# Performance work log

Hardware: AMD Instinct MI355X
Metric: run time of the kernel (lower is better)

## Reference

```python
import jax, jax.numpy as jnp
import numpy as np
import math

B, D, NH, NS, NT = 16, 256, 512, 8, 32
NV = NS * NT          # 256 prediction variables
L, H, A = 4, 8, 64    # attention layers, heads, head dim
HA = H * A            # 512
M = 512               # mlp_dim
R = 128               # resolution
EPS = 1e-5


def setup_inputs() -> dict:
    key = jax.random.key(0)
    ks = jax.random.split(key, 32)
    s = 0.02
    inp = {
        'hist_encoded': jax.random.normal(ks[0], (B, NH, D), jnp.float32),
        'hist_true_u': jax.random.uniform(ks[1], (B, NH), jnp.float32),
        'pred_encoded': jax.random.normal(ks[2], (B, NV, D), jnp.float32),
        'pred_true_u': jax.random.uniform(ks[3], (B, NV), jnp.float32),
        # dimension shifting layer
        'ds_w': jax.random.normal(ks[4], (D, HA), jnp.float32) * s,
        'ds_b': jnp.zeros((HA,), jnp.float32),
        # per-layer, per-head key/value creators: Linear(D+1 -> A)
        'key_w': jax.random.normal(ks[5], (L, H, D + 1, A), jnp.float32) * s,
        'key_b': jnp.zeros((L, H, A), jnp.float32),
        'val_w': jax.random.normal(ks[6], (L, H, D + 1, A), jnp.float32) * s,
        'val_b': jnp.zeros((L, H, A), jnp.float32),
        # layer norms
        'ln1_g': jnp.ones((L, HA), jnp.float32),
        'ln1_b': jnp.zeros((L, HA), jnp.float32),
        'ln2_g': jnp.ones((L, HA), jnp.float32),
        'ln2_b': jnp.zeros((L, HA), jnp.float32),
        # feed-forward (mlp_layers=2): HA->M, M->M, M->HA
        'ff_w1': jax.random.normal(ks[7], (L, HA, M), jnp.float32) * s,
        'ff_b1': jnp.zeros((L, M), jnp.float32),
        'ff_w2': jax.random.normal(ks[8], (L, M, M), jnp.float32) * s,
        'ff_b2': jnp.zeros((L, M), jnp.float32),
        'ff_w3': jax.random.normal(ks[9], (L, M, HA), jnp.float32) * s,
        'ff_b3': jnp.zeros((L, HA), jnp.float32),
        # dist extractor
        'de_w': jax.random.normal(ks[10], (HA, R), jnp.float32) * s,
        'de_b': jnp.zeros((R,), jnp.float32),
        'num_series': NS,
        'num_timesteps': NT,
    }
    return inp


def _ln(x, g, b):
    m = x.mean(-1, keepdims=True)
    v = ((x - m) ** 2).mean(-1, keepdims=True)
    return g * (x - m) / jnp.sqrt(v + EPS) + b


def _forward(hist_encoded, hist_true_u, pred_encoded, pred_true_u,
             ds_w, ds_b, key_w, key_b, val_w, val_b,
             ln1_g, ln1_b, ln2_g, ln2_b,
             ff_w1, ff_b1, ff_w2, ff_b2, ff_w3, ff_b3,
             de_w, de_b):
    Bm, NVm, Dm = pred_encoded.shape
    NHm = hist_encoded.shape[1]
    Lm, Hm, _, Am = key_w.shape
    W = NHm + NVm
    # identity permutation in the source loss() -> no-op
    att = pred_encoded @ ds_w + ds_b  # [B, NV, HA]
    # key/value inputs: [hist||u ; pred||u] -> [B, W, D+1]
    ki = jnp.concatenate([
        jnp.concatenate([hist_encoded, hist_true_u[:, :, None]], axis=2),
        jnp.concatenate([pred_encoded, pred_true_u[:, :, None]], axis=2)], axis=1)
    keys = jnp.einsum('bwd,lhda->lbhwa', ki, key_w) + key_b[:, None, :, None, :]
    vals = jnp.einsum('bwd,lhda->lbhwa', ki, val_w) + val_b[:, None, :, None, :]
    # flipped-triangular mask: position w is masked iff w >= NH + v
    mask = jnp.arange(W)[None, :] >= (NHm + jnp.arange(NVm)[:, None])  # [NV, W]
    scale = Am ** (-0.5)
    for l in range(Lm):
        avh = att.reshape(Bm, NVm, Hm, Am)
        prod = jnp.einsum('bvhi,bhwi->bhvw', avh, keys[l])  # [B,H,NV,W]
        prod = jnp.where(mask, -jnp.inf, prod) * scale
        w = jax.nn.softmax(prod, axis=-1)
        a = jnp.einsum('bhvw,bhwj->bvhj', w, vals[l]).reshape(Bm, NVm, Hm * Am)
        att = _ln(att + a, ln1_g[l], ln1_b[l])
        ff = jnp.maximum(att @ ff_w1[l] + ff_b1[l], 0.0)
        ff = jnp.maximum(ff @ ff_w2[l] + ff_b2[l], 0.0)
        ff = ff @ ff_w3[l] + ff_b3[l]
        att = _ln(att + ff, ln2_g[l], ln2_b[l])
    res = de_w.shape[-1]
    target = jnp.clip(jnp.floor(pred_true_u[:, 1:] * res).astype(jnp.int32), 0, res - 1)
    logits = (att @ de_w + de_b)[:, 1:, :]
    lp = math.log(res) + jax.nn.log_softmax(logits, axis=2)
    lp = jnp.take_along_axis(lp, target[:, :, None], axis=2)[:, :, 0]
    return -lp.sum(axis=1)  # [B]


def reference(hist_encoded, hist_true_u, pred_encoded, pred_true_u,
              ds_w, ds_b, key_w, key_b, val_w, val_b,
              ln1_g, ln1_b, ln2_g, ln2_b,
              ff_w1, ff_b1, ff_w2, ff_b2, ff_w3, ff_b3,
              de_w, de_b, num_series, num_timesteps):
    assert pred_encoded.shape[1] == num_series * num_timesteps
    return _forward(hist_encoded, hist_true_u, pred_encoded, pred_true_u,
                    ds_w, ds_b, key_w, key_b, val_w, val_b,
                    ln1_g, ln1_b, ln2_g, ln2_b,
                    ff_w1, ff_b1, ff_w2, ff_b2, ff_w3, ff_b3,
                    de_w, de_b)
```

## Files before the change

### kernel.cpp

```cpp
#include <hip/hip_runtime.h>

constexpr int kB = 16, kD = 256, kNH = 512, kNV = 256, kW = 768;
constexpr int kL = 4, kH = 8, kA = 64, kHA = 512, kM = 512, kR = 128;
constexpr int kKP = 288;
constexpr int kRows = kB * kNV;

typedef __bf16 bf16x8 __attribute__((ext_vector_type(8)));
typedef __bf16 bf16x4 __attribute__((ext_vector_type(4)));
typedef float f32x4 __attribute__((ext_vector_type(4)));

__device__ inline void load_lds16(const __bf16* g, __bf16* l) {
  __builtin_amdgcn_global_load_lds(
      (const __attribute__((address_space(1))) void*)g,
      (__attribute__((address_space(3))) void*)l, 16, 0, 0);
}

constexpr int kP1 = kB * kW * kKP;
constexpr int kP2 = 4096 * kKP;
constexpr int kP3 = 12 * 512 * 512;
constexpr int kP4 = 200704;
constexpr int kP5 = 16;
constexpr int kPT = kP1 + kP2 + kP3 + kP4 + kP5;

__global__ void prep_kernel(const float* __restrict__ hist,
                            const float* __restrict__ hist_u,
                            const float* __restrict__ pred,
                            const float* __restrict__ pred_u,
                            const float* __restrict__ kw,
                            const float* __restrict__ vw,
                            const float* __restrict__ w1,
                            const float* __restrict__ w2,
                            const float* __restrict__ w3,
                            const float* __restrict__ ds_w,
                            const float* __restrict__ de_w,
                            const float* __restrict__ key_b,
                            const float* __restrict__ val_b,
                            __bf16* __restrict__ ki,
                            __bf16* __restrict__ kvwt,
                            __bf16* __restrict__ ffwt,
                            __bf16* __restrict__ ds_wt,
                            __bf16* __restrict__ de_wt,
                            float* __restrict__ kvb,
                            float* __restrict__ outz) {
  int i = blockIdx.x * 256 + threadIdx.x;
  if (i < kP1) {
    int d = i % kKP;
    int bw = i / kKP;
    int w = bw % kW;
    int b = bw / kW;
    float v = 0.f;
    if (d < 257) {
      if (w < kNH)
        v = (d < kD) ? hist[((size_t)b * kNH + w) * kD + d] : hist_u[b * kNH + w];
      else {
        int p = w - kNH;
        v = (d < kD) ? pred[((size_t)b * kNV + p) * kD + d] : pred_u[b * kNV + p];
      }
    }
    ki[i] = (__bf16)v;
  } else if (i < kP1 + kP2) {
    int j = i - kP1;
    int d = j % kKP;
    int c = j / kKP;
    float v = 0.f;
    if (d < 257) {
      bool isv = c >= 2048;
      int cc = isv ? c - 2048 : c;
      int l = cc >> 9, rest = cc & 511;
      int h = rest >> 6, a = rest & 63;
      size_t src = (((size_t)l * kH + h) * 257 + d) * kA + a;
      v = isv ? vw[src] : kw[src];
    }
    kvwt[j] = (__bf16)v;
  } else if (i < kP1 + kP2 + kP3) {
    int j = i - kP1 - kP2;
    int k = j & 511;
    int n = (j >> 9) & 511;
    int mat = j >> 18;
    int l = mat / 3, which = mat % 3;
    const float* src = which == 0 ? w1 : which == 1 ? w2 : w3;
    ffwt[j] = (__bf16)src[((size_t)l * 512 + k) * 512 + n];
  } else if (i < kP1 + kP2 + kP3 + kP4) {
    int j = i - kP1 - kP2 - kP3;
    if (j < 131072) {
      int n = j >> 8, k = j & 255;
      ds_wt[j] = (__bf16)ds_w[k * 512 + n];
    } else if (j < 196608) {
      int jj = j - 131072;
      int n = jj >> 9, k = jj & 511;
      de_wt[jj] = (__bf16)de_w[k * 128 + n];
    } else {
      int c = j - 196608;
      bool isv = c >= 2048;
      int cc = isv ? c - 2048 : c;
      int l = cc >> 9, rest = cc & 511;
      kvb[c] = isv ? val_b[l * 512 + rest] : key_b[l * 512 + rest];
    }
  } else if (i < kPT) {
    outz[i - kP1 - kP2 - kP3 - kP4] = 0.f;
  }
}

template <int BN, int OMODE, bool RELU, bool KIMAP, bool BIASROW>
__device__ __forceinline__ void gemm_core(
    int bxv, int byv, const __bf16* __restrict__ A,
    const __bf16* __restrict__ Bt, const float* __restrict__ bias,
    void* __restrict__ Cout, __bf16* __restrict__ Cout2, int K, int lda,
    int ldc, __bf16* Sm) {
  constexpr int JN = BN / 32;
  constexpr int BROWS = BN / 4;
  constexpr int SSTEP = (128 + BN) * 32;
  const int t = threadIdx.x;
  const int wid = t >> 6;
  const int lane = t & 63;
  const int bm = byv * 128;
  const int bn = bxv * BN;
  const int wm = (wid >> 1) * 64;
  const int wn = (wid & 1) * (BN / 2);
  const int sr = lane >> 2, sc = lane & 3;
  const int skey = (sr >> 1) & 3;
  const int abase = KIMAP ? ((bm >> 8) * 768 + 512 + (bm & 255)) : bm;
  const __bf16* Ag = A + (size_t)(abase + wid * 32 + sr) * lda + (sc ^ skey) * 8;
  const __bf16* Bg = Bt + (size_t)(bn + wid * BROWS + sr) * K + (sc ^ skey) * 8;
  __bf16* A0 = Sm;
  __bf16* B0 = Sm + 4096;
  __bf16* A1 = Sm + SSTEP;
  __bf16* B1 = Sm + SSTEP + 4096;

  auto stage = [&](int k0, __bf16* As, __bf16* Bs) {
    load_lds16(Ag + k0, As + (wid * 32) * 32);
    load_lds16(Ag + (size_t)16 * lda + k0, As + (wid * 32 + 16) * 32);
    load_lds16(Bg + k0, Bs + (wid * BROWS) * 32);
    if (BN == 128)
      load_lds16(Bg + (size_t)16 * K + k0, Bs + (wid * BROWS + 16) * 32);
  };

  f32x4 acc[4][JN] = {};
  const int q = lane >> 4, mr = lane & 15;
  const int rkey = (mr >> 1) & 3;
  stage(0, A0, B0);
  __syncthreads();
  for (int k0 = 0; k0 < K; k0 += 32) {
    if (k0 + 32 < K) stage(k0 + 32, A1, B1);
    bf16x8 af[4], bfr[JN];
#pragma unroll
    for (int i = 0; i < 4; ++i)
      af[i] = *(const bf16x8*)(A0 + (wm + i * 16 + mr) * 32 + (q ^ rkey) * 8);
#pragma unroll
    for (int j = 0; j < JN; ++j)
      bfr[j] = *(const bf16x8*)(B0 + (wn + j * 16 + mr) * 32 + (q ^ rkey) * 8);
#pragma unroll
    for (int i = 0; i < 4; ++i)
#pragma unroll
      for (int j = 0; j < JN; ++j)
        acc[i][j] = __builtin_amdgcn_mfma_f32_16x16x32_bf16(af[i], bfr[j],
                                                            acc[i][j], 0, 0, 0);
    __syncthreads();
    __bf16* tp = A0; A0 = A1; A1 = tp;
    tp = B0; B0 = B1; B1 = tp;
  }
  if (OMODE == 1) {
    constexpr int PS = BN + 8;
    __bf16* Cs = Sm;
#pragma unroll
    for (int j = 0; j < JN; ++j) {
      float bscol = BIASROW ? 0.f : bias[bn + wn + j * 16 + mr];
#pragma unroll
      for (int i = 0; i < 4; ++i) {
#pragma unroll
        for (int r = 0; r < 4; ++r) {
          float v = acc[i][j][r] +
                    (BIASROW ? bias[bm + wm + i * 16 + q * 4 + r] : bscol);
          if (RELU) v = fmaxf(v, 0.f);
          Cs[(wm + i * 16 + q * 4 + r) * PS + wn + j * 16 + mr] = (__bf16)v;
        }
      }
    }
    __syncthreads();
    constexpr int lpr = BN / 8;
    constexpr int rpi = 512 / BN;
    const int rl = lane / lpr, cl = (lane % lpr) * 8;
#pragma unroll
    for (int it = 0; it < BN / 16; ++it) {
      int row = wid * 32 + it * rpi + rl;
      bf16x8 v = *(const bf16x8*)&Cs[row * PS + cl];
      *(bf16x8*)((__bf16*)Cout + (size_t)(bm + row) * ldc + bn + cl) = v;
    }
  } else {
    constexpr int PSF = BN + 4;
    float* Csf = (float*)Sm;
#pragma unroll
    for (int j = 0; j < JN; ++j) {
      float bscol = bias[bn + wn + j * 16 + mr];
#pragma unroll
      for (int i = 0; i < 4; ++i) {
#pragma unroll
        for (int r = 0; r < 4; ++r) {
          float v = acc[i][j][r] + bscol;
          if (RELU) v = fmaxf(v, 0.f);
          Csf[(wm + i * 16 + q * 4 + r) * PSF + wn + j * 16 + mr] = v;
        }
      }
    }
    __syncthreads();
    const int rl = lane >> 4, cl = (lane & 15) * 4;
#pragma unroll
    for (int it = 0; it < 8; ++it) {
      int row = wid * 32 + it * 4 + rl;
      f32x4 v = *(const f32x4*)&Csf[row * PSF + cl];
      size_t gidx = (size_t)(bm + row) * ldc + bn + cl;
      *(f32x4*)((float*)Cout + gidx) = v;
      bf16x4 vb = {(__bf16)v[0], (__bf16)v[1], (__bf16)v[2], (__bf16)v[3]};
      *(bf16x4*)(Cout2 + gidx) = vb;
    }
  }
}

__global__ __launch_bounds__(256) void gemm3_kernel(
    const __bf16* __restrict__ ki, const __bf16* __restrict__ ds_wt,
    const float* __restrict__ ds_b, float* __restrict__ att,
    __bf16* __restrict__ att_bf, const __bf16* __restrict__ kv_wt,
    const float* __restrict__ kvb, __bf16* __restrict__ kvs_k,
    __bf16* __restrict__ vT) {
  __shared__ __bf16 smem[17408];
  int bid = (blockIdx.x & 7) * 416 + (blockIdx.x >> 3);
  if (bid < 256) {
    gemm_core<64, 2, false, true, false>(bid & 7, bid >> 3, ki, ds_wt, ds_b,
                                         att, att_bf, 256, kKP, 512, smem);
  } else if (bid < 1792) {
    int b2 = bid - 256;
    gemm_core<128, 1, false, false, false>(b2 & 15, b2 >> 4, ki, kv_wt, kvb,
                                           kvs_k, nullptr, kKP, kKP, 2048,
                                           smem);
  } else {
    int b3 = bid - 1792;
    gemm_core<128, 1, false, false, true>(b3 % 96, b3 / 96,
                                          kv_wt + (size_t)2048 * kKP, ki,
                                          kvb + 2048, vT, nullptr, kKP, kKP,
                                          12288, smem);
  }
}

template <bool RELU>
__global__ __launch_bounds__(256) void gemm_ff_kernel(
    const __bf16* __restrict__ A, const __bf16* __restrict__ Bt,
    const float* __restrict__ bias, __bf16* __restrict__ Cout) {
  __shared__ __bf16 smem[12288];
  gemm_core<64, 1, RELU, false, false>(blockIdx.x, blockIdx.y, A, Bt, bias,
                                       Cout, nullptr, 512, 512, 512, smem);
}

__global__ __launch_bounds__(256) void attn_mfma_kernel(
    const __bf16* __restrict__ attbf, const __bf16* __restrict__ kvs_k,
    const __bf16* __restrict__ vT, __bf16* __restrict__ outbf, int l) {
  const int id = blockIdx.x;
  const int kk = id >> 3;
  const int b = ((kk >> 5) << 3) | (id & 7);
  const int qt = kk & 3;
  const int h = (kk >> 2) & 7;
  __shared__ __bf16 Ks[64 * 72];
  __shared__ __bf16 Vt[64 * 72];
  __shared__ __bf16 Ps[64 * 72];
  const int t = threadIdx.x;
  const int w = t >> 6, lane = t & 63;
  const int quad = lane >> 4, mr = lane & 15;
  bf16x8 aq[2];
  {
    const __bf16* qp = attbf + ((size_t)(b * kNV + qt * 64 + w * 16 + mr) * kHA +
                                h * kA + quad * 8);
    aq[0] = *(const bf16x8*)qp;
    aq[1] = *(const bf16x8*)(qp + 32);
  }
  f32x4 o[4] = {};
  float m_ = -1e30f, l_ = 0.f;
  const int cmax = kNH + qt * 64;
  const int pr = t >> 2, pc = t & 3;
  const __bf16* kbase = kvs_k + ((size_t)(b * kW + pr) * 2048 + l * 512 + h * kA);
  const __bf16* vbase = vT + (size_t)(l * 512 + h * kA + pr) * 12288 + b * kW;
  bf16x8 kc0, kc1, vc0, vc1;
  kc0 = *(const bf16x8*)(kbase + pc * 8);
  kc1 = *(const bf16x8*)(kbase + pc * 8 + 32);
  vc0 = *(const bf16x8*)(vbase + pc * 16);
  vc1 = *(const bf16x8*)(vbase + pc * 16 + 8);
  for (int c0 = 0; c0 <= cmax; c0 += 64) {
    __syncthreads();
    *(bf16x8*)&Ks[pr * 72 + pc * 8] = kc0;
    *(bf16x8*)&Ks[pr * 72 + pc * 8 + 32] = kc1;
    *(bf16x8*)&Vt[pr * 72 + pc * 16] = vc0;
    *(bf16x8*)&Vt[pr * 72 + pc * 16 + 8] = vc1;
    __syncthreads();
    if (c0 + 64 <= cmax) {
      const __bf16* kp = kbase + (size_t)(c0 + 64) * 2048;
      const __bf16* vp = vbase + c0 + 64;
      kc0 = *(const bf16x8*)(kp + pc * 8);
      kc1 = *(const bf16x8*)(kp + pc * 8 + 32);
      vc0 = *(const bf16x8*)(vp + pc * 16);
      vc1 = *(const bf16x8*)(vp + pc * 16 + 8);
    }
    f32x4 s[4];
#pragma unroll
    for (int j = 0; j < 4; ++j) {
      bf16x8 ak0 = *(const bf16x8*)&Ks[(j * 16 + mr) * 72 + quad * 8];
      bf16x8 ak1 = *(const bf16x8*)&Ks[(j * 16 + mr) * 72 + quad * 8 + 32];
      f32x4 z = {};
      z = __builtin_amdgcn_mfma_f32_16x16x32_bf16(ak0, aq[0], z, 0, 0, 0);
      z = __builtin_amdgcn_mfma_f32_16x16x32_bf16(ak1, aq[1], z, 0, 0, 0);
      s[j] = z;
    }
    const int lim = cmax - c0;
    float sv[16], mx = -1e30f;
#pragma unroll
    for (int j = 0; j < 4; ++j)
#pragma unroll
      for (int r = 0; r < 4; ++r) {
        int p = j * 16 + quad * 4 + r;
        float x = (p < lim + mr) ? s[j][r] * 0.125f : -1e30f;
        sv[j * 4 + r] = x;
        mx = fmaxf(mx, x);
      }
    mx = fmaxf(mx, __shfl_xor(mx, 16));
    mx = fmaxf(mx, __shfl_xor(mx, 32));
    float mnew = fmaxf(m_, mx);
    float corr = __expf(m_ - mnew);
    float rs = 0.f;
#pragma unroll
    for (int i = 0; i < 16; ++i) {
      sv[i] = __expf(sv[i] - mnew);
      rs += sv[i];
    }
    rs += __shfl_xor(rs, 16);
    rs += __shfl_xor(rs, 32);
    l_ = l_ * corr + rs;
    m_ = mnew;
#pragma unroll
    for (int j = 0; j < 4; ++j) {
      bf16x4 pk = {(__bf16)sv[j * 4 + 0], (__bf16)sv[j * 4 + 1],
                   (__bf16)sv[j * 4 + 2], (__bf16)sv[j * 4 + 3]};
      *(bf16x4*)&Ps[(w * 16 + mr) * 72 + j * 16 + quad * 4] = pk;
    }
#pragma unroll
    for (int r = 0; r < 4; ++r) {
      float cr = __shfl(corr, quad * 4 + r);
#pragma unroll
      for (int j = 0; j < 4; ++j) o[j][r] *= cr;
    }
    bf16x8 ap0 = *(const bf16x8*)&Ps[(w * 16 + mr) * 72 + quad * 8];
    bf16x8 ap1 = *(const bf16x8*)&Ps[(w * 16 + mr) * 72 + quad * 8 + 32];
#pragma unroll
    for (int j = 0; j < 4; ++j) {
      bf16x8 b0 = *(const bf16x8*)&Vt[(j * 16 + mr) * 72 + quad * 8];
      bf16x8 b1 = *(const bf16x8*)&Vt[(j * 16 + mr) * 72 + quad * 8 + 32];
      o[j] = __builtin_amdgcn_mfma_f32_16x16x32_bf16(ap0, b0, o[j], 0, 0, 0);
      o[j] = __builtin_amdgcn_mfma_f32_16x16x32_bf16(ap1, b1, o[j], 0, 0, 0);
    }
  }
  float invl = 1.f / l_;
#pragma unroll
  for (int r = 0; r < 4; ++r) {
    float ir = __shfl(invl, quad * 4 + r);
    int row = b * kNV + qt * 64 + w * 16 + quad * 4 + r;
#pragma unroll
    for (int j = 0; j < 4; ++j)
      outbf[(size_t)row * kHA + h * kA + j * 16 + mr] = (__bf16)(o[j][r] * ir);
  }
}

__global__ __launch_bounds__(128) void add_ln_kernel(
    float* __restrict__ att, const __bf16* __restrict__ addbf,
    const float* __restrict__ g, const float* __restrict__ be,
    __bf16* __restrict__ attbf) {
  const int row = blockIdx.x;
  const int t = threadIdx.x;
  float4* ar = (float4*)(att + (size_t)row * kHA);
  bf16x4 dv = *(const bf16x4*)(addbf + (size_t)row * kHA + t * 4);
  float4 x = ar[t];
  x.x += (float)dv[0]; x.y += (float)dv[1];
  x.z += (float)dv[2]; x.w += (float)dv[3];
  float s = x.x + x.y + x.z + x.w;
  float sq = x.x * x.x + x.y * x.y + x.z * x.z + x.w * x.w;
  for (int o = 32; o; o >>= 1) {
    s += __shfl_xor(s, o);
    sq += __shfl_xor(sq, o);
  }
  __shared__ float red[4];
  if ((t & 63) == 0) { red[(t >> 6) * 2] = s; red[(t >> 6) * 2 + 1] = sq; }
  __syncthreads();
  float S = red[0] + red[2], Q = red[1] + red[3];
  float mean = S * (1.f / kHA);
  float inv = rsqrtf(Q * (1.f / kHA) - mean * mean + 1e-5f);
  float4 gv = ((const float4*)g)[t];
  float4 bv = ((const float4*)be)[t];
  float4 y;
  y.x = gv.x * (x.x - mean) * inv + bv.x;
  y.y = gv.y * (x.y - mean) * inv + bv.y;
  y.z = gv.z * (x.z - mean) * inv + bv.z;
  y.w = gv.w * (x.w - mean) * inv + bv.w;
  ar[t] = y;
  bf16x4 yb = {(__bf16)y.x, (__bf16)y.y, (__bf16)y.z, (__bf16)y.w};
  *(bf16x4*)(attbf + (size_t)row * kHA + t * 4) = yb;
}

__global__ __launch_bounds__(256) void de_loss_kernel(
    const __bf16* __restrict__ attbf, const __bf16* __restrict__ de_wt,
    const float* __restrict__ de_b, const float* __restrict__ pred_u,
    float* __restrict__ out) {
  const int blk = blockIdx.x;
  const int t = threadIdx.x;
  const int w = t >> 6, lane = t & 63, quad = lane >> 4, mr = lane & 15;
  const int row0 = blk * 64 + w * 16;
  f32x4 acc[8] = {};
  const __bf16* Ap = attbf + (size_t)(row0 + mr) * kHA + quad * 8;
#pragma unroll 4
  for (int k0 = 0; k0 < 512; k0 += 32) {
    bf16x8 a = *(const bf16x8*)(Ap + k0);
#pragma unroll
    for (int j = 0; j < 8; ++j) {
      bf16x8 bb =
          *(const bf16x8*)(de_wt + (size_t)(j * 16 + mr) * 512 + k0 + quad * 8);
      acc[j] = __builtin_amdgcn_mfma_f32_16x16x32_bf16(a, bb, acc[j], 0, 0, 0);
    }
  }
  float dbv[8];
#pragma unroll
  for (int j = 0; j < 8; ++j) dbv[j] = de_b[j * 16 + mr];
  float lpacc = 0.f;
#pragma unroll
  for (int r = 0; r < 4; ++r) {
    int row = row0 + quad * 4 + r;
    int v = row & 255;
    float lg[8], mx = -1e30f;
#pragma unroll
    for (int j = 0; j < 8; ++j) {
      lg[j] = acc[j][r] + dbv[j];
      mx = fmaxf(mx, lg[j]);
    }
    mx = fmaxf(mx, __shfl_xor(mx, 1));
    mx = fmaxf(mx, __shfl_xor(mx, 2));
    mx = fmaxf(mx, __shfl_xor(mx, 4));
    mx = fmaxf(mx, __shfl_xor(mx, 8));
    float se = 0.f;
#pragma unroll
    for (int j = 0; j < 8; ++j) se += __expf(lg[j] - mx);
    se += __shfl_xor(se, 1);
    se += __shfl_xor(se, 2);
    se += __shfl_xor(se, 4);
    se += __shfl_xor(se, 8);
    float lse = mx + __logf(se);
    float u = pred_u[(row >> 8) * 256 + v];
    int tgt = (int)floorf(u * 128.f);
    tgt = max(0, min(127, tgt));
    float cand = (mr == (tgt & 15)) ? lg[tgt >> 4] : 0.f;
    cand += __shfl_xor(cand, 1);
    cand += __shfl_xor(cand, 2);
    cand += __shfl_xor(cand, 4);
    cand += __shfl_xor(cand, 8);
    float lp = (v >= 1) ? (4.8520302639196171f + cand - lse) : 0.f;
    lpacc += lp;
  }
  lpacc += __shfl_xor(lpacc, 16);
  lpacc += __shfl_xor(lpacc, 32);
  __shared__ float red[4];
  if (lane == 0) red[w] = lpacc;
  __syncthreads();
  if (t == 0)
    atomicAdd(&out[blk >> 2], -(red[0] + red[1] + red[2] + red[3]));
}

extern "C" void kernel_launch(void* const* d_in, const int* in_sizes, int n_in,
                              void* d_out, int out_size, void* d_ws, size_t ws_size,
                              hipStream_t stream) {
  const float* hist   = (const float*)d_in[0];
  const float* hist_u = (const float*)d_in[1];
  const float* pred   = (const float*)d_in[2];
  const float* pred_u = (const float*)d_in[3];
  const float* ds_w   = (const float*)d_in[4];
  const float* ds_b   = (const float*)d_in[5];
  const float* key_w  = (const float*)d_in[6];
  const float* key_b  = (const float*)d_in[7];
  const float* val_w  = (const float*)d_in[8];
  const float* val_b  = (const float*)d_in[9];
  const float* ln1_g  = (const float*)d_in[10];
  const float* ln1_b  = (const float*)d_in[11];
  const float* ln2_g  = (const float*)d_in[12];
  const float* ln2_b  = (const float*)d_in[13];
  const float* ff_w1  = (const float*)d_in[14];
  const float* ff_b1  = (const float*)d_in[15];
  const float* ff_w2  = (const float*)d_in[16];
  const float* ff_b2  = (const float*)d_in[17];
  const float* ff_w3  = (const float*)d_in[18];
  const float* ff_b3  = (const float*)d_in[19];
  const float* de_w   = (const float*)d_in[20];
  const float* de_b   = (const float*)d_in[21];
  float* out = (float*)d_out;

  char* ws = (char*)d_ws;
  size_t off = 0;
  auto alloc = [&](size_t bytes) { char* p = ws + off; off += bytes; return p; };
  __bf16* ki_bf  = (__bf16*)alloc((size_t)kB * kW * kKP * 2);
  __bf16* kv_wt  = (__bf16*)alloc((size_t)4096 * kKP * 2);
  __bf16* ffw_t  = (__bf16*)alloc((size_t)12 * 512 * 512 * 2);
  __bf16* ds_wt  = (__bf16*)alloc((size_t)512 * 256 * 2);
  __bf16* de_wt  = (__bf16*)alloc((size_t)128 * 512 * 2);
  float*  kvb    = (float*)alloc((size_t)4096 * 4);
  __bf16* kvs_k  = (__bf16*)alloc((size_t)kB * kW * 2048 * 2);
  __bf16* vT     = (__bf16*)alloc((size_t)2048 * 12288 * 2);
  float*  att    = (float*)alloc((size_t)kRows * kHA * 4);
  __bf16* att_bf = (__bf16*)alloc((size_t)kRows * kHA * 2);
  __bf16* tmp_bf = (__bf16*)alloc((size_t)kRows * kHA * 2);
  __bf16* ff1_bf = (__bf16*)alloc((size_t)kRows * kM * 2);
  __bf16* ff2_bf = (__bf16*)alloc((size_t)kRows * kM * 2);

  prep_kernel<<<(kPT + 255) / 256, 256, 0, stream>>>(
      hist, hist_u, pred, pred_u, key_w, val_w, ff_w1, ff_w2, ff_w3, ds_w, de_w,
      key_b, val_b, ki_bf, kv_wt, ffw_t, ds_wt, de_wt, kvb, out);

  gemm3_kernel<<<3328, 256, 0, stream>>>(ki_bf, ds_wt, ds_b, att, att_bf, kv_wt,
                                         kvb, kvs_k, vT);

  for (int l = 0; l < kL; ++l) {
    attn_mfma_kernel<<<512, 256, 0, stream>>>(att_bf, kvs_k, vT, tmp_bf, l);
    add_ln_kernel<<<kRows, 128, 0, stream>>>(att, tmp_bf, ln1_g + l * kHA,
                                             ln1_b + l * kHA, att_bf);
    gemm_ff_kernel<true><<<dim3(kM / 64, kRows / 128), 256, 0, stream>>>(
        att_bf, ffw_t + (size_t)(l * 3) * 262144, ff_b1 + l * kM, ff1_bf);
    gemm_ff_kernel<true><<<dim3(kM / 64, kRows / 128), 256, 0, stream>>>(
        ff1_bf, ffw_t + (size_t)(l * 3 + 1) * 262144, ff_b2 + l * kM, ff2_bf);
    gemm_ff_kernel<false><<<dim3(kHA / 64, kRows / 128), 256, 0, stream>>>(
        ff2_bf, ffw_t + (size_t)(l * 3 + 2) * 262144, ff_b3 + l * kHA, tmp_bf);
    add_ln_kernel<<<kRows, 128, 0, stream>>>(att, tmp_bf, ln2_g + l * kHA,
                                             ln2_b + l * kHA, att_bf);
  }
  de_loss_kernel<<<64, 256, 0, stream>>>(att_bf, de_wt, de_b, pred_u, out);
}
```

Before: 463.1 us.

## Triple-buffer GEMM LDS staging with vmcnt-based waits instead of syncthreads

The shared GEMM core moves from double to triple buffering of the LDS tiles, keeping two k-steps of global-to-LDS loads in flight. Explicit s_waitcnt vmcnt counts plus a raw s_barrier replace __syncthreads, so only the older stage has to land before compute continues. Shared memory grows for both GEMM kernels, which may lower occupancy. The XCD-interleaving block index remap in gemm3 is also dropped in favour of plain blockIdx ordering.

```diff
diff --git a/kernel.cpp b/kernel.cpp
--- a/kernel.cpp
+++ b/kernel.cpp
@@ -110,6 +110,7 @@
   constexpr int JN = BN / 32;
   constexpr int BROWS = BN / 4;
   constexpr int SSTEP = (128 + BN) * 32;
+  constexpr int LPS = (BN == 128) ? 4 : 3;
   const int t = threadIdx.x;
   const int wid = t >> 6;
   const int lane = t & 63;
@@ -122,12 +123,10 @@
   const int abase = KIMAP ? ((bm >> 8) * 768 + 512 + (bm & 255)) : bm;
   const __bf16* Ag = A + (size_t)(abase + wid * 32 + sr) * lda + (sc ^ skey) * 8;
   const __bf16* Bg = Bt + (size_t)(bn + wid * BROWS + sr) * K + (sc ^ skey) * 8;
-  __bf16* A0 = Sm;
-  __bf16* B0 = Sm + 4096;
-  __bf16* A1 = Sm + SSTEP;
-  __bf16* B1 = Sm + SSTEP + 4096;
-
-  auto stage = [&](int k0, __bf16* As, __bf16* Bs) {
+
+  auto stage = [&](int k0, __bf16* buf) {
+    __bf16* As = buf;
+    __bf16* Bs = buf + 4096;
     load_lds16(Ag + k0, As + (wid * 32) * 32);
     load_lds16(Ag + (size_t)16 * lda + k0, As + (wid * 32 + 16) * 32);
     load_lds16(Bg + k0, Bs + (wid * BROWS) * 32);
@@ -138,26 +137,36 @@
   f32x4 acc[4][JN] = {};
   const int q = lane >> 4, mr = lane & 15;
   const int rkey = (mr >> 1) & 3;
-  stage(0, A0, B0);
-  __syncthreads();
-  for (int k0 = 0; k0 < K; k0 += 32) {
-    if (k0 + 32 < K) stage(k0 + 32, A1, B1);
+  const int nst = K >> 5;
+  __bf16* cB = Sm;
+  __bf16* nB = Sm + SSTEP;
+  __bf16* fB = Sm + 2 * SSTEP;
+  stage(0, cB);
+  stage(32, nB);
+  asm volatile("s_waitcnt vmcnt(%0)" ::"n"(LPS) : "memory");
+  __builtin_amdgcn_s_barrier();
+  for (int k = 0; k < nst; ++k) {
+    if (k + 2 < nst) stage((k + 2) << 5, fB);
     bf16x8 af[4], bfr[JN];
 #pragma unroll
     for (int i = 0; i < 4; ++i)
-      af[i] = *(const bf16x8*)(A0 + (wm + i * 16 + mr) * 32 + (q ^ rkey) * 8);
+      af[i] = *(const bf16x8*)(cB + (wm + i * 16 + mr) * 32 + (q ^ rkey) * 8);
 #pragma unroll
     for (int j = 0; j < JN; ++j)
-      bfr[j] = *(const bf16x8*)(B0 + (wn + j * 16 + mr) * 32 + (q ^ rkey) * 8);
+      bfr[j] =
+          *(const bf16x8*)(cB + 4096 + (wn + j * 16 + mr) * 32 + (q ^ rkey) * 8);
 #pragma unroll
     for (int i = 0; i < 4; ++i)
 #pragma unroll
       for (int j = 0; j < JN; ++j)
         acc[i][j] = __builtin_amdgcn_mfma_f32_16x16x32_bf16(af[i], bfr[j],
                                                             acc[i][j], 0, 0, 0);
-    __syncthreads();
-    __bf16* tp = A0; A0 = A1; A1 = tp;
-    tp = B0; B0 = B1; B1 = tp;
+    if (k + 2 < nst)
+      asm volatile("s_waitcnt vmcnt(%0)" ::"n"(LPS) : "memory");
+    else
+      asm volatile("s_waitcnt vmcnt(0)" ::: "memory");
+    __builtin_amdgcn_s_barrier();
+    __bf16* tp = cB; cB = nB; nB = fB; fB = tp;
   }
   if (OMODE == 1) {
     constexpr int PS = BN + 8;
@@ -222,8 +231,8 @@
     __bf16* __restrict__ att_bf, const __bf16* __restrict__ kv_wt,
     const float* __restrict__ kvb, __bf16* __restrict__ kvs_k,
     __bf16* __restrict__ vT) {
-  __shared__ __bf16 smem[17408];
-  int bid = (blockIdx.x & 7) * 416 + (blockIdx.x >> 3);
+  __shared__ __bf16 smem[24576];
+  int bid = blockIdx.x;
   if (bid < 256) {
     gemm_core<64, 2, false, true, false>(bid & 7, bid >> 3, ki, ds_wt, ds_b,
                                          att, att_bf, 256, kKP, 512, smem);
@@ -245,7 +254,7 @@
 __global__ __launch_bounds__(256) void gemm_ff_kernel(
     const __bf16* __restrict__ A, const __bf16* __restrict__ Bt,
     const float* __restrict__ bias, __bf16* __restrict__ Cout) {
-  __shared__ __bf16 smem[12288];
+  __shared__ __bf16 smem[18432];
   gemm_core<64, 1, RELU, false, false>(blockIdx.x, blockIdx.y, A, Bt, bias,
                                        Cout, nullptr, 512, 512, 512, smem);
 }
```

Result: faster. 442.7 us (-4.4%).
